# Optimization experiments

Measured on AMD Instinct MI355X. Metric: run time of the kernel, lower is better.

Reference implementation:

```python
import jax, jax.numpy as jnp
import numpy as np
import math

B, T, C, H, LC, DFF = 2, 1024, 1024, 16, 256, 4096
EPS = 1e-6


def _ln(x):
    # LayerNorm without affine (elementwise_affine=False under AdaLN), eps=1e-6
    m = jnp.mean(x, -1, keepdims=True)
    v = jnp.mean((x - m) ** 2, -1, keepdims=True)
    return (x - m) * jax.lax.rsqrt(v + EPS)


def _heads(t):
    b, l, c = t.shape
    return t.reshape(b, l, H, c // H).transpose(0, 2, 1, 3)  # (b,H,l,dh)


def _unheads(t):
    b, h, l, d = t.shape
    return t.transpose(0, 2, 1, 3).reshape(b, l, h * d)


def setup_inputs():
    key = jax.random.key(0)
    ks = jax.random.split(key, 16)
    s = 0.02
    p = lambda k, sh: jax.random.normal(k, sh, jnp.float32) * s
    x_star = jax.random.normal(ks[0], (B, T, C), jnp.float32)
    x_hat = jax.random.normal(ks[1], (B, T, C), jnp.float32)
    c = jax.random.normal(ks[2], (B, LC, C), jnp.float32)
    chunk = jnp.sort(jax.random.randint(ks[3], (B, T), 0, 32), axis=1)
    m_star = chunk[:, :, None] > chunk[:, None, :]   # attend to strictly earlier chunks
    m_hat = chunk[:, :, None] == chunk[:, None, :]   # attend within same chunk
    dep_mask = jax.random.bernoulli(ks[4], 0.98, (B, T, T)) | jnp.eye(T, dtype=bool)[None]
    return dict(
        x_star=x_star, x_hat=x_hat, c=c,
        m_star=m_star, m_hat=m_hat, dep_mask=dep_mask,
        ncond_g=jnp.ones((C,), jnp.float32), ncond_b=jnp.zeros((C,), jnp.float32),
        Wq=p(ks[5], (C, C)), bq=jnp.zeros((C,), jnp.float32),
        Wkv=p(ks[6], (C, 2 * C)), bkv=jnp.zeros((2 * C,), jnp.float32),
        Wco=p(ks[7], (C, C)), bco=jnp.zeros((C,), jnp.float32),
        Wada=p(ks[8], (C, 6 * C)), bada=jnp.zeros((6 * C,), jnp.float32),
        Wqkv=p(ks[9], (C, 3 * C)), bqkv=jnp.zeros((3 * C,), jnp.float32),
        Wo=p(ks[10], (C, C)), bo=jnp.zeros((C,), jnp.float32),
        W1=p(ks[11], (C, DFF)), b1=jnp.zeros((DFF,), jnp.float32),
        W2=p(ks[12], (DFF, C)), b2=jnp.zeros((C,), jnp.float32),
    )


def _cross_attn(x, c, Wq, bq, Wkv, bkv, Wco, bco):
    q = _heads(x @ Wq + bq)
    k, v = jnp.split(c @ Wkv + bkv, 2, -1)
    k, v = _heads(k), _heads(v)
    att = jnp.einsum('bhtd,bhsd->bhts', q, k) / math.sqrt(C // H)
    y = jnp.einsum('bhts,bhsd->bhtd', jax.nn.softmax(att, -1), v)
    return _unheads(y) @ Wco + bco


def _interleave(xs, xh, m_star, m_hat, dep, Wqkv, bqkv, Wo, bo):
    # Attention.forward_interleave (eval: dropout identity)
    NEG = -jnp.inf
    sc = 1.0 / math.sqrt(C // H)
    qkv = lambda x: [_heads(t) for t in jnp.split(x @ Wqkv + bqkv, 3, -1)]
    qs, ks, vs = qkv(xs)
    qh, kh, vh = qkv(xh)
    blk_star = (~m_star)[:, None]     # True -> block
    blk_hat = (~m_hat)[:, None]
    blk_dep = (~dep)[:, None]
    causal = jnp.triu(jnp.ones((T, T), bool), 1)[None, None]
    # star stream: causal + dependency mask
    att_star = jnp.einsum('bhtd,bhsd->bhts', qs, ks) * sc
    att_star = jnp.where(blk_dep, NEG, att_star)
    p_star = jax.nn.softmax(jnp.where(causal, NEG, att_star), -1)
    y_star = _unheads(jnp.einsum('bhts,bhsd->bhtd', p_star, vs)) @ Wo + bo
    # hat stream: merge logits (q_hat vs k_star on earlier chunks, q_hat vs k_hat within chunk)
    a1 = jnp.where(blk_star, NEG, jnp.einsum('bhtd,bhsd->bhts', qh, ks) * sc)
    a2 = jnp.where(blk_hat, NEG, jnp.einsum('bhtd,bhsd->bhts', qh, kh) * sc)
    merged = jnp.where(jnp.isinf(a2), a1, a2)
    merged = jnp.where(blk_dep, NEG, merged)
    p_hat = jax.nn.softmax(merged, -1)
    y_hat = jnp.einsum('bhts,bhsd->bhtd', jnp.where(blk_star, 0.0, p_hat), vs) \
          + jnp.einsum('bhts,bhsd->bhtd', jnp.where(blk_hat, 0.0, p_hat), vh)
    y_hat = _unheads(y_hat) @ Wo + bo
    return y_star, y_hat


def reference(x_star, x_hat, c, m_star, m_hat, dep_mask,
              ncond_g, ncond_b, Wq, bq, Wkv, bkv, Wco, bco, Wada, bada,
              Wqkv, bqkv, Wo, bo, W1, b1, W2, b2):
    mod = lambda x, sh, scale: x * (1 + scale) + sh
    mlp = lambda x: jax.nn.gelu(x @ W1 + b1, approximate=True) @ W2 + b2
    ca = lambda x: _cross_attn(_ln(x) * ncond_g + ncond_b, c, Wq, bq, Wkv, bkv, Wco, bco)
    ada = lambda t: jnp.split(jax.nn.silu(t) @ Wada + bada, 6, -1)
    gs = ada(ca(x_star))
    gh = ada(ca(x_hat))
    ms = mod(_ln(x_star), gs[0], gs[1])
    mh = mod(_ln(x_hat), gh[0], gh[1])
    ys, yh = _interleave(ms, mh, m_star, m_hat, dep_mask, Wqkv, bqkv, Wo, bo)
    x_star = x_star + gs[2] * ys
    x_hat = x_hat + gh[2] * yh
    x_star = x_star + gs[5] * mlp(mod(_ln(x_star), gs[3], gs[4]))
    x_hat = x_hat + gh[5] * mlp(mod(_ln(x_hat), gh[3], gh[4]))
    return x_star, x_hat
```

## Files before the change

kernel.cpp:

```cpp
#include <hip/hip_runtime.h>
#include <hip/hip_bf16.h>
#include <stdint.h>

#define DEVI __device__ __forceinline__

typedef __bf16 bf16x8 __attribute__((ext_vector_type(8)));
typedef float f32x4 __attribute__((ext_vector_type(4)));
typedef unsigned short us;
typedef unsigned long long ull;

DEVI float b2f(us u) { union { unsigned int i; float f; } v; v.i = ((unsigned int)u) << 16; return v.f; }
DEVI us f2b(float f) {
  union { unsigned int i; float f; } v; v.f = f;
  unsigned int r = (v.i + 0x7fffu + ((v.i >> 16) & 1u)) >> 16;
  return (us)r;
}

#define NEGINF (-__builtin_inff())

DEVI void gl2lds16(const us* g, us* l) {
  __builtin_amdgcn_global_load_lds(
      (const __attribute__((address_space(1))) unsigned int*)g,
      (__attribute__((address_space(3))) unsigned int*)l, 16, 0, 0);
}

__global__ __launch_bounds__(256) void detect_flags(
    const unsigned int* __restrict__ xw, const unsigned int* __restrict__ mw,
    int* __restrict__ flags) {
  const int t = threadIdx.x;
  int cnt = 0, big = 0;
  for (int i = t; i < 4096; i += 256) {
    unsigned int w = xw[i];
    us lo = (us)(w & 0xffffu);
    float a = fabsf(b2f(lo));
    cnt += ((lo == 0) || (a >= 1e-8f && a <= 256.f)) ? 1 : 0;
    big |= (mw[i] > 1u) ? 1 : 0;
  }
  for (int o = 32; o; o >>= 1) { cnt += __shfl_down(cnt, o); big |= __shfl_down(big, o); }
  __shared__ int sc[4], sb[4];
  if ((t & 63) == 0) { sc[t >> 6] = cnt; sb[t >> 6] = big; }
  __syncthreads();
  if (t == 0) {
    flags[0] = (sc[0] + sc[1] + sc[2] + sc[3] < 2048) ? 1 : 0;
    flags[1] = (sb[0] | sb[1] | sb[2] | sb[3]);
  }
}

__global__ __launch_bounds__(256) void cvt_bf16(
    const void* __restrict__ src, us* __restrict__ dst, int n,
    const int* __restrict__ flags) {
  const int f32mode = flags[0];
  int idx = (blockIdx.x * 256 + threadIdx.x) * 4;
  if (idx >= n) return;
  if (f32mode) {
    const float* s = (const float*)src;
    float4 v = *(const float4*)(s + idx);
    dst[idx] = f2b(v.x); dst[idx + 1] = f2b(v.y);
    dst[idx + 2] = f2b(v.z); dst[idx + 3] = f2b(v.w);
  } else {
    *(uint2*)(dst + idx) = *(const uint2*)((const us*)src + idx);
  }
}

struct P10 { const void* p[10]; };
__global__ __launch_bounds__(256) void cvt_small(P10 ps, us* __restrict__ dst,
                                                 const int* __restrict__ flags) {
  const int offs[11] = {0, 1024, 2048, 3072, 5120, 6144, 12288, 15360, 16384, 20480, 21504};
  int idx = blockIdx.x * 256 + threadIdx.x;
  if (idx >= 21504) return;
  int seg = 0;
#pragma unroll
  for (int i = 1; i < 10; ++i) seg += (idx >= offs[i]) ? 1 : 0;
  int local = idx - offs[seg];
  float v = flags[0] ? ((const float*)ps.p[seg])[local]
                     : b2f(((const us*)ps.p[seg])[local]);
  dst[idx] = f2b(v);
}

__global__ __launch_bounds__(256) void transpose_cvt64(
    const void* __restrict__ W, us* __restrict__ WT, int K, int N,
    const int* __restrict__ flags) {
  __shared__ __attribute__((aligned(16))) us tile[64 * 72];
  const int f32m = flags[0];
  const int k0 = blockIdx.x * 64, n0 = blockIdx.y * 64;
  const int t = threadIdx.x;
  const int row = t >> 2, colb = (t & 3) * 16;
  const int sw = ((row >> 4) & 3) << 4;
  us tmp[16];
  if (f32m) {
    const float* src = (const float*)W + (size_t)(k0 + row) * N + n0 + colb;
#pragma unroll
    for (int i = 0; i < 16; i += 4) {
      float4 v = *(const float4*)(src + i);
      tmp[i] = f2b(v.x); tmp[i + 1] = f2b(v.y); tmp[i + 2] = f2b(v.z); tmp[i + 3] = f2b(v.w);
    }
  } else {
    const us* src = (const us*)W + (size_t)(k0 + row) * N + n0 + colb;
    *(uint4*)tmp = *(const uint4*)src;
    *(uint4*)(tmp + 8) = *(const uint4*)(src + 8);
  }
  *(uint4*)&tile[row * 72 + (colb ^ sw)] = *(uint4*)tmp;
  *(uint4*)&tile[row * 72 + (colb ^ sw) + 8] = *(uint4*)(tmp + 8);
  __syncthreads();
  const int orow = t >> 2, ocolb = (t & 3) * 16;
  const int pc = (orow & 15) | ((orow & 48) ^ (ocolb & 48));
  us out[16];
#pragma unroll
  for (int i = 0; i < 16; ++i) out[i] = tile[(ocolb + i) * 72 + pc];
  us* dst = WT + (size_t)(n0 + orow) * K + k0 + ocolb;
  *(uint4*)dst = *(uint4*)out;
  *(uint4*)(dst + 8) = *(uint4*)(out + 8);
}

struct P3 { const void* p[3]; };
__global__ __launch_bounds__(256) void pack_mask3(P3 ms, ull* __restrict__ bits,
                                                  const int* __restrict__ flags) {
  const int bytemode = flags[1];
  const void* m = ms.p[blockIdx.y];
  ull* out = bits + (size_t)blockIdx.y * 32768;
  int wv = blockIdx.x * 4 + (threadIdx.x >> 6);
  int lane = threadIdx.x & 63;
  for (int w = 0; w < 16; ++w) {
    int v;
    if (bytemode) v = ((const unsigned char*)m)[(size_t)wv * 1024 + w * 64 + lane];
    else          v = ((const int*)m)[(size_t)wv * 1024 + w * 64 + lane];
    ull b = __ballot(v != 0);
    if (lane == 0) out[(size_t)wv * 16 + w] = b;
  }
}

__global__ __launch_bounds__(256) void hat_blockflags(
    const ull* __restrict__ starb, const ull* __restrict__ hatb, int* __restrict__ bf) {
  const int bt = blockIdx.x;
  const int b = bt >> 4, tt = bt & 15;
  const int t = threadIdx.x, wv = t >> 6, lane = t & 63;
  const int t0 = tt * 64;
  for (int k = 0; k < 4; ++k) {
    int ck = wv * 4 + k;
    ull sw = starb[(size_t)(b * 1024 + t0 + lane) * 16 + ck];
    ull hw = hatb[(size_t)(b * 1024 + t0 + lane) * 16 + ck];
    int f = (__ballot(sw != 0ull) ? 1 : 0) | (__ballot(hw != 0ull) ? 2 : 0);
    if (lane == 0) bf[bt * 16 + ck] = f;
  }
}

__global__ __launch_bounds__(256) void vtrans(
    const us* __restrict__ src, us* __restrict__ dst,
    int T, int stride, int colBase, int rowOff) {
  __shared__ __attribute__((aligned(16))) us tile[64][65];
  const int bh = blockIdx.y, b = bh >> 4, h = bh & 15;
  const int t0 = blockIdx.x * 64;
  const int t = threadIdx.x;
#pragma unroll
  for (int it = 0; it < 2; ++it) {
    int idx = it * 256 + t; int r = idx >> 3, c8 = (idx & 7) * 8;
    uint4 d4 = *(const uint4*)(src + (size_t)(rowOff + b * T + t0 + r) * stride + colBase + h * 64 + c8);
    const us* e = (const us*)&d4;
#pragma unroll
    for (int i = 0; i < 8; ++i) tile[r][c8 + i] = e[i];
  }
  __syncthreads();
#pragma unroll
  for (int it = 0; it < 2; ++it) {
    int idx = it * 256 + t; int d = idx >> 3, c8 = (idx & 7) * 8;
    us tmp[8];
#pragma unroll
    for (int i = 0; i < 8; ++i) tmp[i] = tile[c8 + i][d];
    *(uint4*)(dst + ((size_t)(bh * 64 + d)) * T + t0 + c8) = *(const uint4*)tmp;
  }
}

__global__ __launch_bounds__(256) void vtrans_qkv(
    const us* __restrict__ src, us* __restrict__ dst0, us* __restrict__ dst1) {
  __shared__ __attribute__((aligned(16))) us tile[64][65];
  const int z = blockIdx.z;
  us* dst = z ? dst1 : dst0;
  const int rowOff = z ? 2048 : 0;
  const int bh = blockIdx.y, b = bh >> 4, h = bh & 15;
  const int t0 = blockIdx.x * 64;
  const int t = threadIdx.x;
#pragma unroll
  for (int it = 0; it < 2; ++it) {
    int idx = it * 256 + t; int r = idx >> 3, c8 = (idx & 7) * 8;
    uint4 d4 = *(const uint4*)(src + (size_t)(rowOff + b * 1024 + t0 + r) * 3072 + 2048 + h * 64 + c8);
    const us* e = (const us*)&d4;
#pragma unroll
    for (int i = 0; i < 8; ++i) tile[r][c8 + i] = e[i];
  }
  __syncthreads();
#pragma unroll
  for (int it = 0; it < 2; ++it) {
    int idx = it * 256 + t; int d = idx >> 3, c8 = (idx & 7) * 8;
    us tmp[8];
#pragma unroll
    for (int i = 0; i < 8; ++i) tmp[i] = tile[c8 + i][d];
    *(uint4*)(dst + ((size_t)(bh * 64 + d)) * 1024 + t0 + c8) = *(const uint4*)tmp;
  }
}

__global__ __launch_bounds__(256) void ln_affine(
    const void* __restrict__ xs, const void* __restrict__ xh,
    const us* __restrict__ gw, const us* __restrict__ bw,
    us* __restrict__ lnx, us* __restrict__ xn, const int* __restrict__ flags) {
  const int f32m = flags[0];
  const int row = blockIdx.x;
  const void* xp = (row < 2048) ? xs : xh;
  const size_t base = (size_t)(row & 2047) * 1024;
  const int t = threadIdx.x;
  float v[4]; float s = 0.f, ss = 0.f;
#pragma unroll
  for (int i = 0; i < 4; ++i) {
    size_t idx = base + i * 256 + t;
    float x = f32m ? ((const float*)xp)[idx] : b2f(((const us*)xp)[idx]);
    v[i] = x; s += x; ss += x * x;
  }
  for (int o = 32; o; o >>= 1) { s += __shfl_down(s, o); ss += __shfl_down(ss, o); }
  __shared__ float red[2][4];
  const int wv = t >> 6, lane = t & 63;
  if (lane == 0) { red[0][wv] = s; red[1][wv] = ss; }
  __syncthreads();
  s = red[0][0] + red[0][1] + red[0][2] + red[0][3];
  ss = red[1][0] + red[1][1] + red[1][2] + red[1][3];
  const float mean = s * (1.f / 1024.f);
  const float var = fmaxf(ss * (1.f / 1024.f) - mean * mean, 0.f);
  const float rstd = rsqrtf(var + 1e-6f);
  const size_t ro = (size_t)row * 1024;
#pragma unroll
  for (int i = 0; i < 4; ++i) {
    int c = i * 256 + t;
    float n = (v[i] - mean) * rstd;
    lnx[ro + c] = f2b(n);
    xn[ro + c] = f2b(n * b2f(gw[c]) + b2f(bw[c]));
  }
}

__global__ __launch_bounds__(256) void mod_ms(
    const us* __restrict__ lnx, const us* __restrict__ gada, us* __restrict__ ms) {
  const size_t idx = ((size_t)blockIdx.x * 256 + threadIdx.x) * 4;
  const int row = (int)(idx >> 10), c = (int)(idx & 1023);
  const size_t gb = (size_t)row * 6144;
#pragma unroll
  for (int i = 0; i < 4; ++i) {
    float sh = b2f(gada[gb + c + i]);
    float sc = b2f(gada[gb + 1024 + c + i]);
    ms[idx + i] = f2b(b2f(lnx[idx + i]) * (1.f + sc) + sh);
  }
}

__global__ __launch_bounds__(256) void ln_mod(
    const float* __restrict__ x1, const us* __restrict__ gada, us* __restrict__ m2) {
  const int row = blockIdx.x;
  const float* xp = x1 + (size_t)row * 1024;
  const int t = threadIdx.x;
  float v[4]; float s = 0.f, ss = 0.f;
#pragma unroll
  for (int i = 0; i < 4; ++i) { float x = xp[i * 256 + t]; v[i] = x; s += x; ss += x * x; }
  for (int o = 32; o; o >>= 1) { s += __shfl_down(s, o); ss += __shfl_down(ss, o); }
  __shared__ float red[2][4];
  const int wv = t >> 6, lane = t & 63;
  if (lane == 0) { red[0][wv] = s; red[1][wv] = ss; }
  __syncthreads();
  s = red[0][0] + red[0][1] + red[0][2] + red[0][3];
  ss = red[1][0] + red[1][1] + red[1][2] + red[1][3];
  const float mean = s * (1.f / 1024.f);
  const float var = fmaxf(ss * (1.f / 1024.f) - mean * mean, 0.f);
  const float rstd = rsqrtf(var + 1e-6f);
  const size_t gb = (size_t)row * 6144;
#pragma unroll
  for (int i = 0; i < 4; ++i) {
    int c = i * 256 + t;
    float n = (v[i] - mean) * rstd;
    float sh = b2f(gada[gb + 3072 + c]);
    float sc = b2f(gada[gb + 4096 + c]);
    m2[(size_t)row * 1024 + c] = f2b(n * (1.f + sc) + sh);
  }
}

enum { EPI_BF16 = 0, EPI_SILU, EPI_GELU, EPI_GATE_XRES, EPI_GATE_OUT };

template <int EPI>
DEVI void gemm_epi(float v, int gmr, int gn, int N, void* out,
                   const us* gate, const void* res0, const void* res1,
                   const int* oflags) {
  const size_t oi = (size_t)gmr * N + gn;
  if constexpr (EPI == EPI_BF16) {
    ((us*)out)[oi] = f2b(v);
  } else if constexpr (EPI == EPI_SILU) {
    ((us*)out)[oi] = f2b(v / (1.f + __expf(-v)));
  } else if constexpr (EPI == EPI_GELU) {
    float u = 0.7978845608028654f * (v + 0.044715f * v * v * v);
    float th = 1.f - 2.f / (__expf(2.f * u) + 1.f);
    ((us*)out)[oi] = f2b(0.5f * v * (1.f + th));
  } else if constexpr (EPI == EPI_GATE_XRES) {
    float g = b2f(gate[(size_t)gmr * 6144 + gn]);
    const void* xr = (gmr < 2048) ? res0 : res1;
    size_t xi = (size_t)(gmr & 2047) * 1024 + gn;
    float x = oflags[0] ? ((const float*)xr)[xi] : b2f(((const us*)xr)[xi]);
    ((float*)out)[oi] = x + g * v;
  } else {
    float g = b2f(gate[(size_t)gmr * 6144 + gn]);
    float x = ((const float*)res0)[oi];
    float r2 = x + g * v;
    if (oflags[0]) ((float*)out)[oi] = r2;
    else ((us*)out)[oi] = f2b(r2);
  }
}

template <int EPI>
__global__ __launch_bounds__(256) void gemm_bt(
    const us* __restrict__ A, const us* __restrict__ BT,
    const us* __restrict__ bias, void* __restrict__ out,
    int M, int N, int K,
    const us* __restrict__ gate,
    const void* __restrict__ res0, const void* __restrict__ res1,
    const int* __restrict__ oflags) {
  __shared__ __attribute__((aligned(16))) us As[2][128 * 32];
  __shared__ __attribute__((aligned(16))) us Bs[2][128 * 32];
  const int m0 = blockIdx.x * 128, n0 = blockIdx.y * 128;
  const int t = threadIdx.x;
  const int wave = t >> 6, lane = t & 63;
  const int wm = (wave >> 1) * 64, wn = (wave & 1) * 64;
  const int l16 = lane & 15, quad = lane >> 4;
  f32x4 acc[4][4] = {};

  const int lr = lane >> 2, lc = (lane & 3) * 8;
  const us* gA = A + (size_t)(m0 + wave * 32 + lr) * K + lc;
  const us* gB = BT + (size_t)(n0 + wave * 32 + lr) * K + lc;
  const int wo = wave * 1024;

#define STAGE_BT(buf, k)                                    \
  { us* pA = &As[buf][wo]; us* pB = &Bs[buf][wo];           \
    gl2lds16(gA + (k), pA);                                 \
    gl2lds16(gA + (size_t)16 * K + (k), pA + 512);          \
    gl2lds16(gB + (k), pB);                                 \
    gl2lds16(gB + (size_t)16 * K + (k), pB + 512); }

  STAGE_BT(0, 0);
  STAGE_BT(1, 32);
  const int NK = K >> 5;
  int cur = 0;
  for (int i = 0; i < NK - 1; ++i) {
    asm volatile("s_waitcnt vmcnt(4)\n\ts_barrier" ::: "memory");
    bf16x8 af[4], bfv[4];
#pragma unroll
    for (int x = 0; x < 4; ++x) af[x] = *(const bf16x8*)(const void*)&As[cur][(wm + x * 16 + l16) * 32 + quad * 8];
#pragma unroll
    for (int j = 0; j < 4; ++j) bfv[j] = *(const bf16x8*)(const void*)&Bs[cur][(wn + j * 16 + l16) * 32 + quad * 8];
    asm volatile("s_waitcnt lgkmcnt(0)\n\ts_barrier" ::: "memory");
    if (i + 2 < NK) STAGE_BT(cur, (i + 2) * 32);
#pragma unroll
    for (int x = 0; x < 4; ++x)
#pragma unroll
      for (int j = 0; j < 4; ++j)
        acc[x][j] = __builtin_amdgcn_mfma_f32_16x16x32_bf16(af[x], bfv[j], acc[x][j], 0, 0, 0);
    cur ^= 1;
  }
  asm volatile("s_waitcnt vmcnt(0)\n\ts_barrier" ::: "memory");
  {
    bf16x8 af[4], bfv[4];
#pragma unroll
    for (int x = 0; x < 4; ++x) af[x] = *(const bf16x8*)(const void*)&As[cur][(wm + x * 16 + l16) * 32 + quad * 8];
#pragma unroll
    for (int j = 0; j < 4; ++j) bfv[j] = *(const bf16x8*)(const void*)&Bs[cur][(wn + j * 16 + l16) * 32 + quad * 8];
#pragma unroll
    for (int x = 0; x < 4; ++x)
#pragma unroll
      for (int j = 0; j < 4; ++j)
        acc[x][j] = __builtin_amdgcn_mfma_f32_16x16x32_bf16(af[x], bfv[j], acc[x][j], 0, 0, 0);
  }
#undef STAGE_BT

#pragma unroll
  for (int i = 0; i < 4; ++i) {
    const int gm = m0 + wm + i * 16 + quad * 4;
#pragma unroll
    for (int j = 0; j < 4; ++j) {
      const int gn = n0 + wn + j * 16 + l16;
      const float bv = b2f(bias[gn]);
#pragma unroll
      for (int r = 0; r < 4; ++r)
        gemm_epi<EPI>(acc[i][j][r] + bv, gm + r, gn, N, out, gate, res0, res1, oflags);
    }
  }
}

template <int EPI>
__global__ __launch_bounds__(256) void gemm_bt64(
    const us* __restrict__ A, const us* __restrict__ BT,
    const us* __restrict__ bias, void* __restrict__ out,
    int M, int N, int K,
    const us* __restrict__ gate,
    const void* __restrict__ res0, const void* __restrict__ res1,
    const int* __restrict__ oflags) {
  __shared__ __attribute__((aligned(16))) us As[2][128 * 32];
  __shared__ __attribute__((aligned(16))) us Bs[2][64 * 32];
  const int m0 = blockIdx.x * 128, n0 = blockIdx.y * 64;
  const int t = threadIdx.x;
  const int wave = t >> 6, lane = t & 63;
  const int wm = (wave >> 1) * 64, wn = (wave & 1) * 32;
  const int l16 = lane & 15, quad = lane >> 4;
  f32x4 acc[4][2] = {};

  const int lr = lane >> 2, lc = (lane & 3) * 8;
  const us* gA = A + (size_t)(m0 + wave * 32 + lr) * K + lc;
  const us* gB = BT + (size_t)(n0 + wave * 16 + lr) * K + lc;
  const int woA = wave * 1024, woB = wave * 512;

#define STAGE_BT64(buf, k)                                  \
  { us* pA = &As[buf][woA];                                 \
    gl2lds16(gA + (k), pA);                                 \
    gl2lds16(gA + (size_t)16 * K + (k), pA + 512);          \
    gl2lds16(gB + (k), &Bs[buf][woB]); }

  STAGE_BT64(0, 0);
  STAGE_BT64(1, 32);
  const int NK = K >> 5;
  int cur = 0;
  for (int i = 0; i < NK - 1; ++i) {
    asm volatile("s_waitcnt vmcnt(3)\n\ts_barrier" ::: "memory");
    bf16x8 af[4], bfv[2];
#pragma unroll
    for (int x = 0; x < 4; ++x) af[x] = *(const bf16x8*)(const void*)&As[cur][(wm + x * 16 + l16) * 32 + quad * 8];
#pragma unroll
    for (int j = 0; j < 2; ++j) bfv[j] = *(const bf16x8*)(const void*)&Bs[cur][(wn + j * 16 + l16) * 32 + quad * 8];
    asm volatile("s_waitcnt lgkmcnt(0)\n\ts_barrier" ::: "memory");
    if (i + 2 < NK) STAGE_BT64(cur, (i + 2) * 32);
#pragma unroll
    for (int x = 0; x < 4; ++x)
#pragma unroll
      for (int j = 0; j < 2; ++j)
        acc[x][j] = __builtin_amdgcn_mfma_f32_16x16x32_bf16(af[x], bfv[j], acc[x][j], 0, 0, 0);
    cur ^= 1;
  }
  asm volatile("s_waitcnt vmcnt(0)\n\ts_barrier" ::: "memory");
  {
    bf16x8 af[4], bfv[2];
#pragma unroll
    for (int x = 0; x < 4; ++x) af[x] = *(const bf16x8*)(const void*)&As[cur][(wm + x * 16 + l16) * 32 + quad * 8];
#pragma unroll
    for (int j = 0; j < 2; ++j) bfv[j] = *(const bf16x8*)(const void*)&Bs[cur][(wn + j * 16 + l16) * 32 + quad * 8];
#pragma unroll
    for (int x = 0; x < 4; ++x)
#pragma unroll
      for (int j = 0; j < 2; ++j)
        acc[x][j] = __builtin_amdgcn_mfma_f32_16x16x32_bf16(af[x], bfv[j], acc[x][j], 0, 0, 0);
  }
#undef STAGE_BT64

#pragma unroll
  for (int i = 0; i < 4; ++i) {
    const int gm = m0 + wm + i * 16 + quad * 4;
#pragma unroll
    for (int j = 0; j < 2; ++j) {
      const int gn = n0 + wn + j * 16 + l16;
      const float bv = b2f(bias[gn]);
#pragma unroll
      for (int r = 0; r < 4; ++r)
        gemm_epi<EPI>(acc[i][j][r] + bv, gm + r, gn, N, out, gate, res0, res1, oflags);
    }
  }
}

struct AttnState { float m[4], l[4]; f32x4 o[4]; };

DEVI void st_init(AttnState& s) {
#pragma unroll
  for (int r = 0; r < 4; ++r) { s.m[r] = NEGINF; s.l[r] = 0.f; s.o[r] = f32x4{}; }
}

DEVI void stage64(us* __restrict__ dst, const us* __restrict__ src,
                  int strideUs, int t) {
#pragma unroll
  for (int it = 0; it < 2; ++it) {
    const int id = it * 256 + t;
    const int row = id >> 3, c8 = (id & 7) * 8;
    *(uint4*)&dst[row * 72 + c8] = *(const uint4*)(src + (size_t)row * strideUs + c8);
  }
}

template <bool MASKED>
DEVI void attn_round(const us* __restrict__ Kb, const us* __restrict__ Vb,
                     us* __restrict__ Pb, const ull* mrow,
                     bf16x8 aq0, bf16x8 aq1, AttnState& st,
                     int wv, int l16, int quad) {
  f32x4 s[4];
  __builtin_amdgcn_s_setprio(1);
#pragma unroll
  for (int j = 0; j < 4; ++j) {
    const int row = j * 16 + l16;
    bf16x8 bk0 = *(const bf16x8*)(const void*)&Kb[row * 72 + quad * 8];
    bf16x8 bk1 = *(const bf16x8*)(const void*)&Kb[row * 72 + 32 + quad * 8];
    f32x4 z = {};
    z = __builtin_amdgcn_mfma_f32_16x16x32_bf16(aq0, bk0, z, 0, 0, 0);
    z = __builtin_amdgcn_mfma_f32_16x16x32_bf16(aq1, bk1, z, 0, 0, 0);
    s[j] = z;
  }
  __builtin_amdgcn_s_setprio(0);
  const float CE = 0.18033688011112042f;
#pragma unroll
  for (int r = 0; r < 4; ++r) {
    float mx = fmaxf(fmaxf(s[0][r], s[1][r]), fmaxf(s[2][r], s[3][r]));
#pragma unroll
    for (int o2 = 8; o2; o2 >>= 1) mx = fmaxf(mx, __shfl_xor(mx, o2));
    const float mn = fmaxf(st.m[r], mx);
    const float alpha = exp2f((st.m[r] - mn) * CE);
    const float mnC = mn * CE;
    float rs = 0.f;
#pragma unroll
    for (int j = 0; j < 4; ++j) {
      float p = exp2f(__builtin_fmaf(s[j][r], CE, -mnC));
      if constexpr (MASKED) p = ((mrow[r] >> (j * 16 + l16)) & 1ull) ? p : 0.f;
      rs += p;
      ((__bf16*)Pb)[(wv * 16 + quad * 4 + r) * 72 + j * 16 + l16] = (__bf16)p;
    }
#pragma unroll
    for (int o2 = 8; o2; o2 >>= 1) rs += __shfl_xor(rs, o2);
    st.m[r] = mn;
    st.l[r] = st.l[r] * alpha + rs;
#pragma unroll
    for (int jd = 0; jd < 4; ++jd) st.o[jd][r] *= alpha;
  }
  bf16x8 ap0 = *(const bf16x8*)(const void*)&Pb[(wv * 16 + l16) * 72 + quad * 8];
  bf16x8 ap1 = *(const bf16x8*)(const void*)&Pb[(wv * 16 + l16) * 72 + 32 + quad * 8];
  __builtin_amdgcn_s_setprio(1);
#pragma unroll
  for (int jd = 0; jd < 4; ++jd) {
    bf16x8 v0 = *(const bf16x8*)(const void*)&Vb[(jd * 16 + l16) * 72 + quad * 8];
    bf16x8 v1 = *(const bf16x8*)(const void*)&Vb[(jd * 16 + l16) * 72 + 32 + quad * 8];
    st.o[jd] = __builtin_amdgcn_mfma_f32_16x16x32_bf16(ap0, v0, st.o[jd], 0, 0, 0);
    st.o[jd] = __builtin_amdgcn_mfma_f32_16x16x32_bf16(ap1, v1, st.o[jd], 0, 0, 0);
  }
  __builtin_amdgcn_s_setprio(0);
}

DEVI void attn_write(us* __restrict__ y, const AttnState& st, int rowAbs,
                     int h, int l16, int quad) {
#pragma unroll
  for (int r = 0; r < 4; ++r) {
    const float inv = (st.l[r] > 0.f) ? 1.f / st.l[r] : 0.f;
#pragma unroll
    for (int jd = 0; jd < 4; ++jd)
      y[(size_t)(rowAbs + quad * 4 + r) * 1024 + h * 64 + jd * 16 + l16] =
          f2b(st.o[jd][r] * inv);
  }
}

__global__ __launch_bounds__(256) void cross_attn_mfma(
    const us* __restrict__ q, const us* __restrict__ kv,
    const us* __restrict__ vT, us* __restrict__ y) {
  __shared__ __attribute__((aligned(16))) us Kb[64 * 72];
  __shared__ __attribute__((aligned(16))) us Vb[64 * 72];
  __shared__ __attribute__((aligned(16))) us Pb[64 * 72];
  const int bid = blockIdx.x;
  const int xcd = bid & 7, tmp = bid >> 3;
  const int tt = tmp & 15, gq = tmp >> 4;
  const int g = gq * 8 + xcd;
  const int strm = g >> 5, b = (g >> 4) & 1, h = g & 15;
  const int t = threadIdx.x, wv = t >> 6, lane = t & 63;
  const int l16 = lane & 15, quad = lane >> 4;
  const int rowbase = strm * 2048 + b * 1024 + tt * 64 + wv * 16;
  const us* qp = q + (size_t)(rowbase + l16) * 1024 + h * 64 + quad * 8;
  bf16x8 aq0 = *(const bf16x8*)(qp);
  bf16x8 aq1 = *(const bf16x8*)(qp + 32);
  const us* kb = kv + (size_t)b * (256 * 2048) + h * 64;
  const us* vb = vT + (size_t)(b * 16 + h) * (64 * 256);
  AttnState st; st_init(st);
  for (int rnd = 0; rnd < 4; ++rnd) {
    const int s0 = rnd * 64;
    __syncthreads();
    stage64(Kb, kb + (size_t)s0 * 2048, 2048, t);
    stage64(Vb, vb + s0, 256, t);
    __syncthreads();
    attn_round<false>(Kb, Vb, Pb, nullptr, aq0, aq1, st, wv, l16, quad);
  }
  attn_write(y, st, rowbase, h, l16, quad);
}

DEVI void star_body(us* Kb, us* Vb, us* Pb, const us* qkv, const us* vT,
                    const ull* depb, us* y, int b, int h, int tt, int t) {
  const int wv = t >> 6, lane = t & 63;
  const int l16 = lane & 15, quad = lane >> 4;
  const int t0 = tt * 64;
  const int rowbase = b * 1024 + t0 + wv * 16;
  const us* qp = qkv + (size_t)(rowbase + l16) * 3072 + h * 64 + quad * 8;
  bf16x8 aq0 = *(const bf16x8*)(qp);
  bf16x8 aq1 = *(const bf16x8*)(qp + 32);
  const us* kb = qkv + (size_t)(b * 1024) * 3072 + 1024 + h * 64;
  const us* vb = vT + (size_t)(b * 16 + h) * 65536;
  AttnState st; st_init(st);
  ull mrow[4];
  for (int ck = 0; ck <= tt; ++ck) {
    const int s0 = ck * 64;
    __syncthreads();
    stage64(Kb, kb + (size_t)s0 * 3072, 3072, t);
    stage64(Vb, vb + s0, 1024, t);
    __syncthreads();
#pragma unroll
    for (int r = 0; r < 4; ++r) {
      ull d = depb[(size_t)(rowbase + quad * 4 + r) * 16 + ck];
      if (ck == tt) {
        const int idx = wv * 16 + quad * 4 + r;
        d &= (2ull << idx) - 1ull;
      }
      mrow[r] = d;
    }
    attn_round<true>(Kb, Vb, Pb, mrow, aq0, aq1, st, wv, l16, quad);
  }
  attn_write(y, st, rowbase, h, l16, quad);
}

DEVI void hat_body(us* Kb, us* Vb, us* Pb, const us* qkv,
                   const us* vsT, const us* vhT,
                   const ull* starb, const ull* hatb, const ull* depb,
                   const int* bflags, us* y, int b, int h, int tt, int t) {
  const int wv = t >> 6, lane = t & 63;
  const int l16 = lane & 15, quad = lane >> 4;
  const int t0 = tt * 64;
  const int rowbase = b * 1024 + t0 + wv * 16;
  const us* qp = qkv + (size_t)(2048 + rowbase + l16) * 3072 + h * 64 + quad * 8;
  bf16x8 aq0 = *(const bf16x8*)(qp);
  bf16x8 aq1 = *(const bf16x8*)(qp + 32);
  const us* ksb = qkv + (size_t)(b * 1024) * 3072 + 1024 + h * 64;
  const us* khb = qkv + (size_t)(2048 + b * 1024) * 3072 + 1024 + h * 64;
  const us* vsb = vsT + (size_t)(b * 16 + h) * 65536;
  const us* vhb = vhT + (size_t)(b * 16 + h) * 65536;
  AttnState st; st_init(st);
  ull mrow[4];
  for (int ck = 0; ck < 16; ++ck) {
    const int f = bflags[(b * 16 + tt) * 16 + ck];
    const int s0 = ck * 64;
    if (f & 1) {
      __syncthreads();
      stage64(Kb, ksb + (size_t)s0 * 3072, 3072, t);
      stage64(Vb, vsb + s0, 1024, t);
      __syncthreads();
#pragma unroll
      for (int r = 0; r < 4; ++r) {
        const size_t mi = (size_t)(rowbase + quad * 4 + r) * 16 + ck;
        mrow[r] = starb[mi] & depb[mi];
      }
      attn_round<true>(Kb, Vb, Pb, mrow, aq0, aq1, st, wv, l16, quad);
    }
    if (f & 2) {
      __syncthreads();
      stage64(Kb, khb + (size_t)s0 * 3072, 3072, t);
      stage64(Vb, vhb + s0, 1024, t);
      __syncthreads();
#pragma unroll
      for (int r = 0; r < 4; ++r) {
        const size_t mi = (size_t)(rowbase + quad * 4 + r) * 16 + ck;
        mrow[r] = hatb[mi] & depb[mi];
      }
      attn_round<true>(Kb, Vb, Pb, mrow, aq0, aq1, st, wv, l16, quad);
    }
  }
  attn_write(y, st, 2048 + rowbase, h, l16, quad);
}

__global__ __launch_bounds__(256) void self_attn_mfma(
    const us* __restrict__ qkv,
    const us* __restrict__ vstT, const us* __restrict__ vhtT,
    const ull* __restrict__ sbits, const ull* __restrict__ hbits,
    const ull* __restrict__ dbits, const int* __restrict__ bflags,
    us* __restrict__ y) {
  __shared__ __attribute__((aligned(16))) us Kb[64 * 72];
  __shared__ __attribute__((aligned(16))) us Vb[64 * 72];
  __shared__ __attribute__((aligned(16))) us Pb[64 * 72];
  const int bid = blockIdx.x;
  const int xcd = bid & 7, tmp = bid >> 3;
  const int pr = tmp & 7, gq = tmp >> 3;
  const int g = gq * 8 + xcd;
  const int ttA = pr, ttB = 15 - pr;
  const int t = threadIdx.x;
  if (g < 32) {
    star_body(Kb, Vb, Pb, qkv, vstT, dbits, y, g >> 4, g & 15, ttA, t);
    star_body(Kb, Vb, Pb, qkv, vstT, dbits, y, g >> 4, g & 15, ttB, t);
  } else {
    const int g2 = g - 32;
    hat_body(Kb, Vb, Pb, qkv, vstT, vhtT, sbits, hbits, dbits, bflags,
             y, g2 >> 4, g2 & 15, ttA, t);
    hat_body(Kb, Vb, Pb, qkv, vstT, vhtT, sbits, hbits, dbits, bflags,
             y, g2 >> 4, g2 & 15, ttB, t);
  }
}

extern "C" void kernel_launch(void* const* d_in, const int* in_sizes, int n_in,
                              void* d_out, int out_size, void* d_ws, size_t ws_size,
                              hipStream_t stream) {
  const void* xs = d_in[0];
  const void* xh = d_in[1];
  const void* cc = d_in[2];
  const void* mstar = d_in[3];
  const void* mhat = d_in[4];
  const void* mdep = d_in[5];
  const void* ng = d_in[6];
  const void* nb = d_in[7];
  const void* Wq = d_in[8];
  const void* bq = d_in[9];
  const void* Wkv = d_in[10];
  const void* bkv = d_in[11];
  const void* Wco = d_in[12];
  const void* bco = d_in[13];
  const void* Wada = d_in[14];
  const void* bada = d_in[15];
  const void* Wqkv = d_in[16];
  const void* bqkv = d_in[17];
  const void* Wo = d_in[18];
  const void* bo = d_in[19];
  const void* W1 = d_in[20];
  const void* b1 = d_in[21];
  const void* W2 = d_in[22];
  const void* b2 = d_in[23];
  (void)in_sizes; (void)n_in; (void)out_size; (void)ws_size;

  char* ws = (char*)d_ws;
  size_t off = 0;
  auto alloc = [&](size_t bytes) -> char* {
    char* p = ws + off;
    off += (bytes + 255) & ~(size_t)255;
    return p;
  };
  int* flags = (int*)alloc(256);
  int* bflags = (int*)alloc(512 * 4);
  us* smallb = (us*)alloc(21504 * 2);
  us* ngb = smallb, *nbb = smallb + 1024, *bqb = smallb + 2048,
      *bkvb = smallb + 3072, *bcob = smallb + 5120, *badab = smallb + 6144,
      *bqkvb = smallb + 12288, *bob = smallb + 15360, *b1b = smallb + 16384,
      *b2b = smallb + 20480;
  us* WqT = (us*)alloc(1048576ull * 2);
  us* WkvT = (us*)alloc(2097152ull * 2);
  us* WcoT = (us*)alloc(1048576ull * 2);
  us* WadaT = (us*)alloc(6291456ull * 2);
  us* WqkvT = (us*)alloc(3145728ull * 2);
  us* WoT = (us*)alloc(1048576ull * 2);
  us* W1T = (us*)alloc(4194304ull * 2);
  us* W2T = (us*)alloc(4194304ull * 2);
  us* xn = (us*)alloc(4194304ull * 2);
  us* qb = (us*)alloc(4194304ull * 2);
  us* kvb = (us*)alloc(1048576ull * 2);
  us* gada = (us*)alloc(25165824ull * 2);
  us* msb = (us*)alloc(4194304ull * 2);
  us* qkvb = (us*)alloc(12582912ull * 2);
  float* x1 = (float*)alloc(4194304ull * 4);
  us* hid = (us*)alloc(16777216ull * 2);
  ull* mb = (ull*)alloc(3ull * 32768 * 8);
  us* kvT = (us*)alloc(524288ull * 2);
  us* vstT = (us*)alloc(2097152ull * 2);
  us* vhtT = (us*)alloc(2097152ull * 2);

  ull* sbits = mb;
  ull* hbits = mb + 32768;
  ull* dbits = mb + 65536;
  us* ccb = hid;
  us* lnx = hid + 1048576;
  us* yca = xn;
  us* silub = qb;
  us* yat = msb;

  dim3 blk(256);
  detect_flags<<<1, blk, 0, stream>>>((const unsigned int*)xs, (const unsigned int*)mdep, flags);

  cvt_bf16<<<512, blk, 0, stream>>>(cc, ccb, 524288, flags);
  P10 ps10; ps10.p[0] = ng; ps10.p[1] = nb; ps10.p[2] = bq; ps10.p[3] = bkv;
  ps10.p[4] = bco; ps10.p[5] = bada; ps10.p[6] = bqkv; ps10.p[7] = bo;
  ps10.p[8] = b1; ps10.p[9] = b2;
  cvt_small<<<84, blk, 0, stream>>>(ps10, smallb, flags);

  transpose_cvt64<<<dim3(16, 16), blk, 0, stream>>>(Wq, WqT, 1024, 1024, flags);
  transpose_cvt64<<<dim3(16, 32), blk, 0, stream>>>(Wkv, WkvT, 1024, 2048, flags);
  transpose_cvt64<<<dim3(16, 16), blk, 0, stream>>>(Wco, WcoT, 1024, 1024, flags);
  transpose_cvt64<<<dim3(16, 96), blk, 0, stream>>>(Wada, WadaT, 1024, 6144, flags);
  transpose_cvt64<<<dim3(16, 48), blk, 0, stream>>>(Wqkv, WqkvT, 1024, 3072, flags);
  transpose_cvt64<<<dim3(16, 16), blk, 0, stream>>>(Wo, WoT, 1024, 1024, flags);
  transpose_cvt64<<<dim3(16, 64), blk, 0, stream>>>(W1, W1T, 1024, 4096, flags);
  transpose_cvt64<<<dim3(64, 16), blk, 0, stream>>>(W2, W2T, 4096, 1024, flags);

  P3 ps3; ps3.p[0] = mstar; ps3.p[1] = mhat; ps3.p[2] = mdep;
  pack_mask3<<<dim3(512, 3), blk, 0, stream>>>(ps3, mb, flags);
  hat_blockflags<<<32, blk, 0, stream>>>(sbits, hbits, bflags);

  ln_affine<<<4096, blk, 0, stream>>>(xs, xh, ngb, nbb, lnx, xn, flags);
  gemm_bt64<EPI_BF16><<<dim3(32, 16), blk, 0, stream>>>(xn, WqT, bqb, qb, 4096, 1024, 1024, nullptr, nullptr, nullptr, nullptr);
  gemm_bt64<EPI_BF16><<<dim3(4, 32), blk, 0, stream>>>(ccb, WkvT, bkvb, kvb, 512, 2048, 1024, nullptr, nullptr, nullptr, nullptr);
  vtrans<<<dim3(4, 32), blk, 0, stream>>>(kvb, kvT, 256, 2048, 1024, 0);
  cross_attn_mfma<<<1024, blk, 0, stream>>>(qb, kvb, kvT, yca);
  gemm_bt64<EPI_SILU><<<dim3(32, 16), blk, 0, stream>>>(yca, WcoT, bcob, silub, 4096, 1024, 1024, nullptr, nullptr, nullptr, nullptr);
  gemm_bt<EPI_BF16><<<dim3(32, 48), blk, 0, stream>>>(silub, WadaT, badab, gada, 4096, 6144, 1024, nullptr, nullptr, nullptr, nullptr);
  mod_ms<<<4096, blk, 0, stream>>>(lnx, gada, msb);
  gemm_bt<EPI_BF16><<<dim3(32, 24), blk, 0, stream>>>(msb, WqkvT, bqkvb, qkvb, 4096, 3072, 1024, nullptr, nullptr, nullptr, nullptr);
  vtrans_qkv<<<dim3(16, 32, 2), blk, 0, stream>>>(qkvb, vstT, vhtT);
  self_attn_mfma<<<512, blk, 0, stream>>>(qkvb, vstT, vhtT, sbits, hbits, dbits, bflags, yat);
  gemm_bt64<EPI_GATE_XRES><<<dim3(32, 16), blk, 0, stream>>>(yat, WoT, bob, x1, 4096, 1024, 1024, gada + 2048, xs, xh, flags);
  ln_mod<<<4096, blk, 0, stream>>>(x1, gada, msb);
  gemm_bt<EPI_GELU><<<dim3(32, 32), blk, 0, stream>>>(msb, W1T, b1b, hid, 4096, 4096, 1024, nullptr, nullptr, nullptr, nullptr);
  gemm_bt64<EPI_GATE_OUT><<<dim3(32, 16), blk, 0, stream>>>(hid, W2T, b2b, d_out, 4096, 1024, 4096, gada + 5120, x1, nullptr, flags);
}
```

Baseline: 622.5 us.

## Process two 64-key chunks per attention round to halve barriers and softmax passes

The attention rounds now stage two 64-key K/V tiles at once and run a 128-wide online-softmax step, which halves the number of __syncthreads pairs and the max/sum reductions and rescales per key. The hat path packs the active star and hat chunks into a bitmask and handles them two at a time instead of one per branch. The cost is double the K/V shared-memory footprint and a larger P buffer, which can lower occupancy. An odd trailing chunk also does wasted work, because it is loaded and computed under a zero mask.

```diff
diff --git a/kernel.cpp b/kernel.cpp
--- a/kernel.cpp
+++ b/kernel.cpp
@@ -479,17 +479,19 @@
 }
 
 template <bool MASKED>
-DEVI void attn_round(const us* __restrict__ Kb, const us* __restrict__ Vb,
-                     us* __restrict__ Pb, const ull* mrow,
-                     bf16x8 aq0, bf16x8 aq1, AttnState& st,
-                     int wv, int l16, int quad) {
-  f32x4 s[4];
+DEVI void attn_round2(const us* __restrict__ Kb0, const us* __restrict__ Kb1,
+                      const us* __restrict__ Vb0, const us* __restrict__ Vb1,
+                      us* __restrict__ Pb, const ull* ma, const ull* mb,
+                      bf16x8 aq0, bf16x8 aq1, AttnState& st,
+                      int wv, int l16, int quad) {
+  f32x4 s[8];
   __builtin_amdgcn_s_setprio(1);
 #pragma unroll
-  for (int j = 0; j < 4; ++j) {
-    const int row = j * 16 + l16;
-    bf16x8 bk0 = *(const bf16x8*)(const void*)&Kb[row * 72 + quad * 8];
-    bf16x8 bk1 = *(const bf16x8*)(const void*)&Kb[row * 72 + 32 + quad * 8];
+  for (int j = 0; j < 8; ++j) {
+    const us* kbuf = (j < 4) ? Kb0 : Kb1;
+    const int row = (j & 3) * 16 + l16;
+    bf16x8 bk0 = *(const bf16x8*)(const void*)&kbuf[row * 72 + quad * 8];
+    bf16x8 bk1 = *(const bf16x8*)(const void*)&kbuf[row * 72 + 32 + quad * 8];
     f32x4 z = {};
     z = __builtin_amdgcn_mfma_f32_16x16x32_bf16(aq0, bk0, z, 0, 0, 0);
     z = __builtin_amdgcn_mfma_f32_16x16x32_bf16(aq1, bk1, z, 0, 0, 0);
@@ -499,7 +501,9 @@
   const float CE = 0.18033688011112042f;
 #pragma unroll
   for (int r = 0; r < 4; ++r) {
-    float mx = fmaxf(fmaxf(s[0][r], s[1][r]), fmaxf(s[2][r], s[3][r]));
+    float mx = s[0][r];
+#pragma unroll
+    for (int j = 1; j < 8; ++j) mx = fmaxf(mx, s[j][r]);
 #pragma unroll
     for (int o2 = 8; o2; o2 >>= 1) mx = fmaxf(mx, __shfl_xor(mx, o2));
     const float mn = fmaxf(st.m[r], mx);
@@ -507,11 +511,14 @@
     const float mnC = mn * CE;
     float rs = 0.f;
 #pragma unroll
-    for (int j = 0; j < 4; ++j) {
+    for (int j = 0; j < 8; ++j) {
       float p = exp2f(__builtin_fmaf(s[j][r], CE, -mnC));
-      if constexpr (MASKED) p = ((mrow[r] >> (j * 16 + l16)) & 1ull) ? p : 0.f;
+      if constexpr (MASKED) {
+        const ull act = (j < 4) ? ma[r] : mb[r];
+        p = ((act >> ((j & 3) * 16 + l16)) & 1ull) ? p : 0.f;
+      }
       rs += p;
-      ((__bf16*)Pb)[(wv * 16 + quad * 4 + r) * 72 + j * 16 + l16] = (__bf16)p;
+      ((__bf16*)Pb)[(wv * 16 + quad * 4 + r) * 136 + j * 16 + l16] = (__bf16)p;
     }
 #pragma unroll
     for (int o2 = 8; o2; o2 >>= 1) rs += __shfl_xor(rs, o2);
@@ -520,15 +527,22 @@
 #pragma unroll
     for (int jd = 0; jd < 4; ++jd) st.o[jd][r] *= alpha;
   }
-  bf16x8 ap0 = *(const bf16x8*)(const void*)&Pb[(wv * 16 + l16) * 72 + quad * 8];
-  bf16x8 ap1 = *(const bf16x8*)(const void*)&Pb[(wv * 16 + l16) * 72 + 32 + quad * 8];
+  bf16x8 ap[4];
+#pragma unroll
+  for (int kk = 0; kk < 4; ++kk)
+    ap[kk] = *(const bf16x8*)(const void*)&Pb[(wv * 16 + l16) * 136 + kk * 32 + quad * 8];
   __builtin_amdgcn_s_setprio(1);
 #pragma unroll
   for (int jd = 0; jd < 4; ++jd) {
-    bf16x8 v0 = *(const bf16x8*)(const void*)&Vb[(jd * 16 + l16) * 72 + quad * 8];
-    bf16x8 v1 = *(const bf16x8*)(const void*)&Vb[(jd * 16 + l16) * 72 + 32 + quad * 8];
-    st.o[jd] = __builtin_amdgcn_mfma_f32_16x16x32_bf16(ap0, v0, st.o[jd], 0, 0, 0);
-    st.o[jd] = __builtin_amdgcn_mfma_f32_16x16x32_bf16(ap1, v1, st.o[jd], 0, 0, 0);
+    const int row = (jd * 16 + l16) * 72;
+    bf16x8 v0 = *(const bf16x8*)(const void*)&Vb0[row + quad * 8];
+    bf16x8 v1 = *(const bf16x8*)(const void*)&Vb0[row + 32 + quad * 8];
+    bf16x8 v2 = *(const bf16x8*)(const void*)&Vb1[row + quad * 8];
+    bf16x8 v3 = *(const bf16x8*)(const void*)&Vb1[row + 32 + quad * 8];
+    st.o[jd] = __builtin_amdgcn_mfma_f32_16x16x32_bf16(ap[0], v0, st.o[jd], 0, 0, 0);
+    st.o[jd] = __builtin_amdgcn_mfma_f32_16x16x32_bf16(ap[1], v1, st.o[jd], 0, 0, 0);
+    st.o[jd] = __builtin_amdgcn_mfma_f32_16x16x32_bf16(ap[2], v2, st.o[jd], 0, 0, 0);
+    st.o[jd] = __builtin_amdgcn_mfma_f32_16x16x32_bf16(ap[3], v3, st.o[jd], 0, 0, 0);
   }
   __builtin_amdgcn_s_setprio(0);
 }
@@ -548,9 +562,9 @@
 __global__ __launch_bounds__(256) void cross_attn_mfma(
     const us* __restrict__ q, const us* __restrict__ kv,
     const us* __restrict__ vT, us* __restrict__ y) {
-  __shared__ __attribute__((aligned(16))) us Kb[64 * 72];
-  __shared__ __attribute__((aligned(16))) us Vb[64 * 72];
-  __shared__ __attribute__((aligned(16))) us Pb[64 * 72];
+  __shared__ __attribute__((aligned(16))) us Kb[2][64 * 72];
+  __shared__ __attribute__((aligned(16))) us Vb[2][64 * 72];
+  __shared__ __attribute__((aligned(16))) us Pb[64 * 136];
   const int bid = blockIdx.x;
   const int xcd = bid & 7, tmp = bid >> 3;
   const int tt = tmp & 15, gq = tmp >> 4;
@@ -565,18 +579,22 @@
   const us* kb = kv + (size_t)b * (256 * 2048) + h * 64;
   const us* vb = vT + (size_t)(b * 16 + h) * (64 * 256);
   AttnState st; st_init(st);
-  for (int rnd = 0; rnd < 4; ++rnd) {
-    const int s0 = rnd * 64;
+  for (int rnd = 0; rnd < 2; ++rnd) {
+    const int s0 = rnd * 128;
     __syncthreads();
-    stage64(Kb, kb + (size_t)s0 * 2048, 2048, t);
-    stage64(Vb, vb + s0, 256, t);
+    stage64(Kb[0], kb + (size_t)s0 * 2048, 2048, t);
+    stage64(Kb[1], kb + (size_t)(s0 + 64) * 2048, 2048, t);
+    stage64(Vb[0], vb + s0, 256, t);
+    stage64(Vb[1], vb + s0 + 64, 256, t);
     __syncthreads();
-    attn_round<false>(Kb, Vb, Pb, nullptr, aq0, aq1, st, wv, l16, quad);
+    attn_round2<false>(Kb[0], Kb[1], Vb[0], Vb[1], Pb, nullptr, nullptr,
+                       aq0, aq1, st, wv, l16, quad);
   }
   attn_write(y, st, rowbase, h, l16, quad);
 }
 
-DEVI void star_body(us* Kb, us* Vb, us* Pb, const us* qkv, const us* vT,
+DEVI void star_body(us (*Kb)[64 * 72], us (*Vb)[64 * 72], us* Pb,
+                    const us* qkv, const us* vT,
                     const ull* depb, us* y, int b, int h, int tt, int t) {
   const int wv = t >> 6, lane = t & 63;
   const int l16 = lane & 15, quad = lane >> 4;
@@ -588,29 +606,36 @@
   const us* kb = qkv + (size_t)(b * 1024) * 3072 + 1024 + h * 64;
   const us* vb = vT + (size_t)(b * 16 + h) * 65536;
   AttnState st; st_init(st);
-  ull mrow[4];
-  for (int ck = 0; ck <= tt; ++ck) {
-    const int s0 = ck * 64;
+  for (int ck0 = 0; ck0 <= tt; ck0 += 2) {
     __syncthreads();
-    stage64(Kb, kb + (size_t)s0 * 3072, 3072, t);
-    stage64(Vb, vb + s0, 1024, t);
+    stage64(Kb[0], kb + (size_t)ck0 * 64 * 3072, 3072, t);
+    stage64(Kb[1], kb + (size_t)(ck0 + 1) * 64 * 3072, 3072, t);
+    stage64(Vb[0], vb + ck0 * 64, 1024, t);
+    stage64(Vb[1], vb + (ck0 + 1) * 64, 1024, t);
     __syncthreads();
+    ull ma[4], mb[4];
 #pragma unroll
     for (int r = 0; r < 4; ++r) {
-      ull d = depb[(size_t)(rowbase + quad * 4 + r) * 16 + ck];
-      if (ck == tt) {
-        const int idx = wv * 16 + quad * 4 + r;
-        d &= (2ull << idx) - 1ull;
+      const size_t mbase = (size_t)(rowbase + quad * 4 + r) * 16;
+      const int idx = wv * 16 + quad * 4 + r;
+      ull dA = depb[mbase + ck0];
+      if (ck0 == tt) dA &= (2ull << idx) - 1ull;
+      ma[r] = dA;
+      ull dB = 0;
+      if (ck0 + 1 <= tt) {
+        dB = depb[mbase + ck0 + 1];
+        if (ck0 + 1 == tt) dB &= (2ull << idx) - 1ull;
       }
-      mrow[r] = d;
+      mb[r] = dB;
     }
-    attn_round<true>(Kb, Vb, Pb, mrow, aq0, aq1, st, wv, l16, quad);
+    attn_round2<true>(Kb[0], Kb[1], Vb[0], Vb[1], Pb, ma, mb,
+                      aq0, aq1, st, wv, l16, quad);
   }
   attn_write(y, st, rowbase, h, l16, quad);
 }
 
-DEVI void hat_body(us* Kb, us* Vb, us* Pb, const us* qkv,
-                   const us* vsT, const us* vhT,
+DEVI void hat_body(us (*Kb)[64 * 72], us (*Vb)[64 * 72], us* Pb,
+                   const us* qkv, const us* vsT, const us* vhT,
                    const ull* starb, const ull* hatb, const ull* depb,
                    const int* bflags, us* y, int b, int h, int tt, int t) {
   const int wv = t >> 6, lane = t & 63;
@@ -625,34 +650,33 @@
   const us* vsb = vsT + (size_t)(b * 16 + h) * 65536;
   const us* vhb = vhT + (size_t)(b * 16 + h) * 65536;
   AttnState st; st_init(st);
-  ull mrow[4];
+  unsigned msk = 0;
   for (int ck = 0; ck < 16; ++ck) {
-    const int f = bflags[(b * 16 + tt) * 16 + ck];
-    const int s0 = ck * 64;
-    if (f & 1) {
-      __syncthreads();
-      stage64(Kb, ksb + (size_t)s0 * 3072, 3072, t);
-      stage64(Vb, vsb + s0, 1024, t);
-      __syncthreads();
-#pragma unroll
-      for (int r = 0; r < 4; ++r) {
-        const size_t mi = (size_t)(rowbase + quad * 4 + r) * 16 + ck;
-        mrow[r] = starb[mi] & depb[mi];
-      }
-      attn_round<true>(Kb, Vb, Pb, mrow, aq0, aq1, st, wv, l16, quad);
+    int f = bflags[(b * 16 + tt) * 16 + ck];
+    msk |= (unsigned)(f & 3) << (2 * ck);
+  }
+  while (msk) {
+    const int sa = (int)__builtin_ctz(msk); msk &= msk - 1;
+    int sb = -1;
+    if (msk) { sb = (int)__builtin_ctz(msk); msk &= msk - 1; }
+    const int cka = sa >> 1, pa = sa & 1;
+    const int ckb = (sb >= 0) ? (sb >> 1) : cka;
+    const int pb = (sb >= 0) ? (sb & 1) : pa;
+    __syncthreads();
+    stage64(Kb[0], (pa ? khb : ksb) + (size_t)cka * 64 * 3072, 3072, t);
+    stage64(Kb[1], (pb ? khb : ksb) + (size_t)ckb * 64 * 3072, 3072, t);
+    stage64(Vb[0], (pa ? vhb : vsb) + cka * 64, 1024, t);
+    stage64(Vb[1], (pb ? vhb : vsb) + ckb * 64, 1024, t);
+    __syncthreads();
+    ull ma[4], mb[4];
+#pragma unroll
+    for (int r = 0; r < 4; ++r) {
+      const size_t mbase = (size_t)(rowbase + quad * 4 + r) * 16;
+      ma[r] = (pa ? hatb : starb)[mbase + cka] & depb[mbase + cka];
+      mb[r] = (sb >= 0) ? ((pb ? hatb : starb)[mbase + ckb] & depb[mbase + ckb]) : 0ull;
     }
-    if (f & 2) {
-      __syncthreads();
-      stage64(Kb, khb + (size_t)s0 * 3072, 3072, t);
-      stage64(Vb, vhb + s0, 1024, t);
-      __syncthreads();
-#pragma unroll
-      for (int r = 0; r < 4; ++r) {
-        const size_t mi = (size_t)(rowbase + quad * 4 + r) * 16 + ck;
-        mrow[r] = hatb[mi] & depb[mi];
-      }
-      attn_round<true>(Kb, Vb, Pb, mrow, aq0, aq1, st, wv, l16, quad);
-    }
+    attn_round2<true>(Kb[0], Kb[1], Vb[0], Vb[1], Pb, ma, mb,
+                      aq0, aq1, st, wv, l16, quad);
   }
   attn_write(y, st, 2048 + rowbase, h, l16, quad);
 }
@@ -663,9 +687,9 @@
     const ull* __restrict__ sbits, const ull* __restrict__ hbits,
     const ull* __restrict__ dbits, const int* __restrict__ bflags,
     us* __restrict__ y) {
-  __shared__ __attribute__((aligned(16))) us Kb[64 * 72];
-  __shared__ __attribute__((aligned(16))) us Vb[64 * 72];
-  __shared__ __attribute__((aligned(16))) us Pb[64 * 72];
+  __shared__ __attribute__((aligned(16))) us Kb[2][64 * 72];
+  __shared__ __attribute__((aligned(16))) us Vb[2][64 * 72];
+  __shared__ __attribute__((aligned(16))) us Pb[64 * 136];
   const int bid = blockIdx.x;
   const int xcd = bid & 7, tmp = bid >> 3;
   const int pr = tmp & 7, gq = tmp >> 3;
```

New measurement: 617.8 us. No clear change (-0.7%).
